# Performance work log

Measured on AMD Instinct MI355X. Metric: run time of the kernel, lower is better.

The kernel has to match this reference:

```python
import jax, jax.numpy as jnp
import numpy as np

N = 65536        # gaussians
NTILE = 8        # tiles per side
TS = 64          # tile size in pixels
T = NTILE * NTILE
K = 256          # depth-sorted gaussians per tile
W = H = NTILE * TS


def setup_inputs() -> dict:
    key = jax.random.key(0)
    ks = jax.random.split(key, 6)
    mu = jax.random.uniform(ks[0], (N, 2), dtype=jnp.float32) * W   # 2D screen means
    L = jax.random.normal(ks[1], (N, 2, 2), dtype=jnp.float32) * 2.0
    # PSD 2x2 covariances with a few-pixel footprint
    cov2d = jnp.einsum('nij,nkj->nik', L, L) + 4.0 * jnp.eye(2, dtype=jnp.float32)
    opacity = jax.random.uniform(ks[2], (N,), dtype=jnp.float32)
    color = jax.random.uniform(ks[3], (N, 3), dtype=jnp.float32)
    depth = jax.random.uniform(ks[4], (N,), dtype=jnp.float32)
    idx = jax.random.randint(ks[5], (T, K), 0, N)
    # depth-sort gaussians within each tile (Screen.depth_sort)
    order = jnp.argsort(depth[idx], axis=1)
    tile_idx = jnp.take_along_axis(idx, order, axis=1).astype(jnp.int32)
    return {"mu": mu, "cov2d": cov2d, "opacity": opacity, "color": color,
            "tile_idx": tile_idx}


def _rasterize(mu, cov2d, opacity, color, tile_idx):
    # closed-form 2x2 inverse of cov2d
    a = cov2d[:, 0, 0]; b = cov2d[:, 0, 1]
    c = cov2d[:, 1, 0]; d = cov2d[:, 1, 1]
    det = jnp.maximum(a * d - b * c, 1e-6)
    inv = jnp.stack([jnp.stack([d, -b], -1),
                     jnp.stack([-c, a], -1)], -2) / det[:, None, None]  # [N,2,2]

    ly, lx = jnp.meshgrid(jnp.arange(TS), jnp.arange(TS), indexing='ij')
    local = (jnp.stack([lx, ly], -1).reshape(TS * TS, 2).astype(jnp.float32)
             + 0.5)  # pixel centers within a tile, [P,2]

    def tile_fn(args):
        tid, idx = args
        ty = tid // NTILE
        tx = tid % NTILE
        origin = jnp.stack([tx * TS, ty * TS]).astype(jnp.float32)
        pix = local + origin                              # [P,2]
        m = mu[idx]                                       # [K,2]
        ic = inv[idx]                                     # [K,2,2]
        op = opacity[idx]                                 # [K]
        col = color[idx]                                  # [K,3]
        dlt = pix[:, None, :] - m[None, :, :]             # [P,K,2]
        maha = jnp.einsum('pki,kij,pkj->pk', dlt, ic, dlt)
        prob = jnp.exp(-0.5 * maha)                       # [P,K]
        alpha = jnp.clip(op[None, :] * prob, 0.01, 0.99)
        # weight_i = alpha_i * (1 - sum_{j<i} alpha_j)  (shifted cumsum, as in source)
        trans = 1.0 - (jnp.cumsum(alpha, axis=1) - alpha)
        w = alpha * trans                                 # [P,K]
        return (w @ col).reshape(TS, TS, 3)

    tiles = jax.lax.map(tile_fn, (jnp.arange(T, dtype=jnp.int32), tile_idx))  # [T,TS,TS,3]
    img = tiles.reshape(NTILE, NTILE, TS, TS, 3)
    img = img.transpose(0, 2, 1, 3, 4).reshape(H, W, 3)
    return img


def reference(mu, cov2d, opacity, color, tile_idx):
    return _rasterize(mu, cov2d, opacity, color, tile_idx)
```

## Files before the change

### kernel.cpp

```cpp
#include <hip/hip_runtime.h>
#include <math.h>

#define TS 64
#define T 64
#define K 256
#define NSEG 4
#define KSEG 64
#define IMG_W 512

__global__ __launch_bounds__(512, 4) void render_all(
    const float* __restrict__ mu, const float* __restrict__ cov,
    const float* __restrict__ opacity, const float* __restrict__ color,
    const int* __restrict__ tile_idx, float* __restrict__ out) {
  __shared__ float4 sA[K];
  __shared__ float4 sB[K];
  __shared__ float sC[K];
  __shared__ float sR[K];
  __shared__ float4 sbuf[2 * K];
  __shared__ float4 sPA[K + 1];
  __shared__ float4 sPK[K + 1];
  __shared__ float sS[NSEG][128][4];
  __shared__ float sD[3][128][4][3];

  int tid = threadIdx.x;
  int blk = blockIdx.x;
  int tile = blk & 63;
  int chunk = blk >> 6;

  if (tid < K) {
    int n = tile_idx[tile * K + tid];
    float a = cov[4 * n + 0];
    float b = cov[4 * n + 1];
    float c = cov[4 * n + 2];
    float d = cov[4 * n + 3];
    float det = fmaxf(a * d - b * c, 1e-6f);
    const float LOG2E = 1.4426950408889634f;
    float s = -0.5f * LOG2E / det;
    float mx = mu[2 * n], my = mu[2 * n + 1];
    float lop = log2f(fmaxf(opacity[n], 1e-30f));
    float cr = color[3 * n], cg = color[3 * n + 1], cb = color[3 * n + 2];
    sA[tid] = make_float4(mx, my, s * d, -s * (b + c));
    sB[tid] = make_float4(s * a, lop, cr, cg);
    sC[tid] = cb;
    float r2 = 1.3862943611f * (lop + 6.6438561898f) * (a + d);
    sR[tid] = r2 * 1.0001f + 1e-3f;
    sbuf[tid] = make_float4(cr, cg, cb, 0.f);
    float fk = (float)tid;
    sbuf[K + tid] = make_float4(fk * cr, fk * cg, fk * cb, 0.f);
  }
  __syncthreads();

  int lane256 = tid & 255;
  float4* mybuf = sbuf + (tid & 256);
  for (int off = 1; off < K; off <<= 1) {
    float4 t;
    bool act = lane256 >= off;
    if (act) t = mybuf[lane256 - off];
    __syncthreads();
    if (act) {
      float4 u = mybuf[lane256];
      mybuf[lane256] = make_float4(u.x + t.x, u.y + t.y, u.z + t.z, 0.f);
    }
    __syncthreads();
  }
  if (tid < K) {
    sPA[tid + 1] = sbuf[tid];
  } else {
    sPK[lane256 + 1] = sbuf[K + lane256];
  }
  if (tid == 0) {
    sPA[0] = make_float4(0.f, 0.f, 0.f, 0.f);
    sPK[0] = make_float4(0.f, 0.f, 0.f, 0.f);
  }
  __syncthreads();

  int seg = __builtin_amdgcn_readfirstlane(tid >> 7);
  int pslot = tid & 127;
  int lx = pslot & 63;
  int bnd = __builtin_amdgcn_readfirstlane(chunk * 2 + ((tid >> 6) & 1));
  int ty = tile >> 3, tx = tile & 7;
  int ly0 = bnd * 4;
  float px = (float)(tx * TS + lx) + 0.5f;
  float py0 = (float)(ty * TS + ly0) + 0.5f;
  const int kb = seg * KSEG;

  unsigned long long m;
  {
    int l = tid & 63;
    float4 Ag = sA[kb + l];
    float r2 = sR[kb + l];
    float x0 = tx * TS + 0.5f, x1 = tx * TS + 63.5f;
    float y0 = py0, y1 = py0 + 3.0f;
    float dxm = fmaxf(fmaxf(Ag.x - x1, x0 - Ag.x), 0.f);
    float dym = fmaxf(fmaxf(Ag.y - y1, y0 - Ag.y), 0.f);
    float d2 = fmaf(dxm, dxm, dym * dym);
    m = __ballot(d2 < r2);
  }

  float C[4][3] = {};
  float An[4][3] = {};
  float Af[3] = {0.f, 0.f, 0.f};
  float S[4] = {};

  int i = kb;
  while (true) {
    int j = (m != 0ULL) ? (kb + (int)__builtin_ctzll(m)) : (kb + KSEG);
    if (j > i) {
      float len = (float)(j - i);
      float4 paj = sPA[j], pai = sPA[i];
      float4 pkj = sPK[j], pki = sPK[i];
      float P1r = paj.x - pai.x, P1g = paj.y - pai.y, P1b = paj.z - pai.z;
      float fi = (float)i;
      float Rr = -1e-4f * fmaf(-fi, P1r, pkj.x - pki.x);
      float Rg = -1e-4f * fmaf(-fi, P1g, pkj.y - pki.y);
      float Rb = -1e-4f * fmaf(-fi, P1b, pkj.z - pki.z);
      Af[0] = fmaf(0.01f, P1r, Af[0]);
      Af[1] = fmaf(0.01f, P1g, Af[1]);
      Af[2] = fmaf(0.01f, P1b, Af[2]);
#pragma unroll
      for (int p = 0; p < 4; ++p) {
        float t = fmaf(-0.01f, S[p], 0.01f);
        C[p][0] = fmaf(t, P1r, C[p][0]) + Rr;
        C[p][1] = fmaf(t, P1g, C[p][1]) + Rg;
        C[p][2] = fmaf(t, P1b, C[p][2]) + Rb;
        S[p] = fmaf(0.01f, len, S[p]);
      }
    }
    if (j >= kb + KSEG) break;
    float4 A4 = sA[j];
    float4 B4 = sB[j];
    float cbv = sC[j];
    float dx = px - A4.x;
    float tb = A4.w * dx;
    float base = fmaf(A4.z * dx, dx, B4.y);
    float dy = py0 - A4.y;
#pragma unroll
    for (int p = 0; p < 4; ++p) {
      float dyp = dy + (float)p;
      float mm = fmaf(dyp, fmaf(B4.x, dyp, tb), base);
      float al =
          __builtin_amdgcn_fmed3f(__builtin_amdgcn_exp2f(mm), 0.01f, 0.99f);
      float w = fmaf(-al, S[p], al);
      C[p][0] = fmaf(w, B4.z, C[p][0]);
      C[p][1] = fmaf(w, B4.w, C[p][1]);
      C[p][2] = fmaf(w, cbv, C[p][2]);
      An[p][0] = fmaf(al, B4.z, An[p][0]);
      An[p][1] = fmaf(al, B4.w, An[p][1]);
      An[p][2] = fmaf(al, cbv, An[p][2]);
      S[p] += al;
    }
    m &= (m - 1ULL);
    i = j + 1;
  }

#pragma unroll
  for (int p = 0; p < 4; ++p) sS[seg][pslot][p] = S[p];
  __syncthreads();

  if (seg >= 1) {
#pragma unroll
    for (int p = 0; p < 4; ++p) {
      float Sp = sS[0][pslot][p];
      if (seg >= 2) Sp += sS[1][pslot][p];
      if (seg >= 3) Sp += sS[2][pslot][p];
      sD[seg - 1][pslot][p][0] = fmaf(-Sp, An[p][0] + Af[0], C[p][0]);
      sD[seg - 1][pslot][p][1] = fmaf(-Sp, An[p][1] + Af[1], C[p][1]);
      sD[seg - 1][pslot][p][2] = fmaf(-Sp, An[p][2] + Af[2], C[p][2]);
    }
  }
  __syncthreads();

  if (seg == 0) {
    int x = tx * TS + lx;
#pragma unroll
    for (int p = 0; p < 4; ++p) {
      int y = ty * TS + ly0 + p;
      size_t o = ((size_t)y * IMG_W + x) * 3;
      out[o + 0] = C[p][0] + sD[0][pslot][p][0] + sD[1][pslot][p][0] +
                   sD[2][pslot][p][0];
      out[o + 1] = C[p][1] + sD[0][pslot][p][1] + sD[1][pslot][p][1] +
                   sD[2][pslot][p][1];
      out[o + 2] = C[p][2] + sD[0][pslot][p][2] + sD[1][pslot][p][2] +
                   sD[2][pslot][p][2];
    }
  }
}

extern "C" void kernel_launch(void* const* d_in, const int* in_sizes, int n_in,
                              void* d_out, int out_size, void* d_ws,
                              size_t ws_size, hipStream_t stream) {
  const float* mu = (const float*)d_in[0];
  const float* cov = (const float*)d_in[1];
  const float* opacity = (const float*)d_in[2];
  const float* color = (const float*)d_in[3];
  const int* tile_idx = (const int*)d_in[4];
  float* out = (float*)d_out;
  (void)d_ws;
  (void)ws_size;

  render_all<<<T * 8, 512, 0, stream>>>(mu, cov, opacity, color, tile_idx,
                                        out);
}
```

Baseline: 68.87 us.

## Replace block-wide shared-memory prefix scan with per-wave shuffle scans

Drops the 8-step block-wide Hillis-Steele scan, which used many __syncthreads, in favour of a per-segment 64-wide wavefront shuffle scan over the color prefixes. Prefix values are then fetched by __shfl inside the gap-accumulation branch instead of being read from shared memory. Work is also split so that the upper 256 threads load colors, with vectorized float4/float2 global loads. The cost is extra shuffle instructions inside the sparse loop and redundant scans across waves.

```diff
diff --git a/kernel.cpp b/kernel.cpp
--- a/kernel.cpp
+++ b/kernel.cpp
@@ -13,12 +13,9 @@
     const float* __restrict__ opacity, const float* __restrict__ color,
     const int* __restrict__ tile_idx, float* __restrict__ out) {
   __shared__ float4 sA[K];
-  __shared__ float4 sB[K];
-  __shared__ float sC[K];
+  __shared__ float2 sB[K];
+  __shared__ float4 sCol[K];
   __shared__ float sR[K];
-  __shared__ float4 sbuf[2 * K];
-  __shared__ float4 sPA[K + 1];
-  __shared__ float4 sPK[K + 1];
   __shared__ float sS[NSEG][128][4];
   __shared__ float sD[3][128][4][3];
 
@@ -27,55 +24,31 @@
   int tile = blk & 63;
   int chunk = blk >> 6;
 
-  if (tid < K) {
-    int n = tile_idx[tile * K + tid];
-    float a = cov[4 * n + 0];
-    float b = cov[4 * n + 1];
-    float c = cov[4 * n + 2];
-    float d = cov[4 * n + 3];
-    float det = fmaxf(a * d - b * c, 1e-6f);
-    const float LOG2E = 1.4426950408889634f;
-    float s = -0.5f * LOG2E / det;
-    float mx = mu[2 * n], my = mu[2 * n + 1];
-    float lop = log2f(fmaxf(opacity[n], 1e-30f));
-    float cr = color[3 * n], cg = color[3 * n + 1], cb = color[3 * n + 2];
-    sA[tid] = make_float4(mx, my, s * d, -s * (b + c));
-    sB[tid] = make_float4(s * a, lop, cr, cg);
-    sC[tid] = cb;
-    float r2 = 1.3862943611f * (lop + 6.6438561898f) * (a + d);
-    sR[tid] = r2 * 1.0001f + 1e-3f;
-    sbuf[tid] = make_float4(cr, cg, cb, 0.f);
-    float fk = (float)tid;
-    sbuf[K + tid] = make_float4(fk * cr, fk * cg, fk * cb, 0.f);
-  }
-  __syncthreads();
-
-  int lane256 = tid & 255;
-  float4* mybuf = sbuf + (tid & 256);
-  for (int off = 1; off < K; off <<= 1) {
-    float4 t;
-    bool act = lane256 >= off;
-    if (act) t = mybuf[lane256 - off];
-    __syncthreads();
-    if (act) {
-      float4 u = mybuf[lane256];
-      mybuf[lane256] = make_float4(u.x + t.x, u.y + t.y, u.z + t.z, 0.f);
-    }
-    __syncthreads();
-  }
-  if (tid < K) {
-    sPA[tid + 1] = sbuf[tid];
-  } else {
-    sPK[lane256 + 1] = sbuf[K + lane256];
-  }
-  if (tid == 0) {
-    sPA[0] = make_float4(0.f, 0.f, 0.f, 0.f);
-    sPK[0] = make_float4(0.f, 0.f, 0.f, 0.f);
+  {
+    int g = tid & 255;
+    int n = tile_idx[tile * K + g];
+    if (tid < K) {
+      float4 cv = *(const float4*)(cov + 4 * n);
+      float2 mm = *(const float2*)(mu + 2 * n);
+      float op = opacity[n];
+      float det = fmaxf(cv.x * cv.w - cv.y * cv.z, 1e-6f);
+      const float LOG2E = 1.4426950408889634f;
+      float s = -0.5f * LOG2E / det;
+      float lop = log2f(fmaxf(op, 1e-30f));
+      sA[g] = make_float4(mm.x, mm.y, s * cv.w, -s * (cv.y + cv.z));
+      sB[g] = make_float2(s * cv.x, lop);
+      float r2 = 1.3862943611f * (lop + 6.6438561898f) * (cv.x + cv.w);
+      sR[g] = r2 * 1.0001f + 1e-3f;
+    } else {
+      const float* cp = color + 3 * n;
+      sCol[g] = make_float4(cp[0], cp[1], cp[2], 0.f);
+    }
   }
   __syncthreads();
 
   int seg = __builtin_amdgcn_readfirstlane(tid >> 7);
   int pslot = tid & 127;
+  int lane = tid & 63;
   int lx = pslot & 63;
   int bnd = __builtin_amdgcn_readfirstlane(chunk * 2 + ((tid >> 6) & 1));
   int ty = tile >> 3, tx = tile & 7;
@@ -84,11 +57,39 @@
   float py0 = (float)(ty * TS + ly0) + 0.5f;
   const int kb = seg * KSEG;
 
+  float icr, icg, icb, jcr, jcg, jcb;
+  {
+    float4 cl = sCol[kb + lane];
+    float fl = (float)lane;
+    icr = cl.x;
+    icg = cl.y;
+    icb = cl.z;
+    jcr = fl * cl.x;
+    jcg = fl * cl.y;
+    jcb = fl * cl.z;
+    for (int off = 1; off < 64; off <<= 1) {
+      float t0 = __shfl_up(icr, off);
+      float t1 = __shfl_up(icg, off);
+      float t2 = __shfl_up(icb, off);
+      float t3 = __shfl_up(jcr, off);
+      float t4 = __shfl_up(jcg, off);
+      float t5 = __shfl_up(jcb, off);
+      if (lane >= off) {
+        icr += t0;
+        icg += t1;
+        icb += t2;
+        jcr += t3;
+        jcg += t4;
+        jcb += t5;
+      }
+    }
+  }
+#define PFX(v, q) ((q) == 0 ? 0.f : __shfl((v), (q)-1))
+
   unsigned long long m;
   {
-    int l = tid & 63;
-    float4 Ag = sA[kb + l];
-    float r2 = sR[kb + l];
+    float4 Ag = sA[kb + lane];
+    float r2 = sR[kb + lane];
     float x0 = tx * TS + 0.5f, x1 = tx * TS + 63.5f;
     float y0 = py0, y1 = py0 + 3.0f;
     float dxm = fmaxf(fmaxf(Ag.x - x1, x0 - Ag.x), 0.f);
@@ -106,14 +107,15 @@
   while (true) {
     int j = (m != 0ULL) ? (kb + (int)__builtin_ctzll(m)) : (kb + KSEG);
     if (j > i) {
-      float len = (float)(j - i);
-      float4 paj = sPA[j], pai = sPA[i];
-      float4 pkj = sPK[j], pki = sPK[i];
-      float P1r = paj.x - pai.x, P1g = paj.y - pai.y, P1b = paj.z - pai.z;
-      float fi = (float)i;
-      float Rr = -1e-4f * fmaf(-fi, P1r, pkj.x - pki.x);
-      float Rg = -1e-4f * fmaf(-fi, P1g, pkj.y - pki.y);
-      float Rb = -1e-4f * fmaf(-fi, P1b, pkj.z - pki.z);
+      int i2 = i - kb, j2 = j - kb;
+      float len = (float)(j2 - i2);
+      float P1r = PFX(icr, j2) - PFX(icr, i2);
+      float P1g = PFX(icg, j2) - PFX(icg, i2);
+      float P1b = PFX(icb, j2) - PFX(icb, i2);
+      float fi = (float)i2;
+      float Rr = -1e-4f * fmaf(-fi, P1r, PFX(jcr, j2) - PFX(jcr, i2));
+      float Rg = -1e-4f * fmaf(-fi, P1g, PFX(jcg, j2) - PFX(jcg, i2));
+      float Rb = -1e-4f * fmaf(-fi, P1b, PFX(jcb, j2) - PFX(jcb, i2));
       Af[0] = fmaf(0.01f, P1r, Af[0]);
       Af[1] = fmaf(0.01f, P1g, Af[1]);
       Af[2] = fmaf(0.01f, P1b, Af[2]);
@@ -128,25 +130,25 @@
     }
     if (j >= kb + KSEG) break;
     float4 A4 = sA[j];
-    float4 B4 = sB[j];
-    float cbv = sC[j];
+    float2 B2 = sB[j];
+    float4 c4 = sCol[j];
     float dx = px - A4.x;
     float tb = A4.w * dx;
-    float base = fmaf(A4.z * dx, dx, B4.y);
+    float base = fmaf(A4.z * dx, dx, B2.y);
     float dy = py0 - A4.y;
 #pragma unroll
     for (int p = 0; p < 4; ++p) {
       float dyp = dy + (float)p;
-      float mm = fmaf(dyp, fmaf(B4.x, dyp, tb), base);
+      float mm = fmaf(dyp, fmaf(B2.x, dyp, tb), base);
       float al =
           __builtin_amdgcn_fmed3f(__builtin_amdgcn_exp2f(mm), 0.01f, 0.99f);
       float w = fmaf(-al, S[p], al);
-      C[p][0] = fmaf(w, B4.z, C[p][0]);
-      C[p][1] = fmaf(w, B4.w, C[p][1]);
-      C[p][2] = fmaf(w, cbv, C[p][2]);
-      An[p][0] = fmaf(al, B4.z, An[p][0]);
-      An[p][1] = fmaf(al, B4.w, An[p][1]);
-      An[p][2] = fmaf(al, cbv, An[p][2]);
+      C[p][0] = fmaf(w, c4.x, C[p][0]);
+      C[p][1] = fmaf(w, c4.y, C[p][1]);
+      C[p][2] = fmaf(w, c4.z, C[p][2]);
+      An[p][0] = fmaf(al, c4.x, An[p][0]);
+      An[p][1] = fmaf(al, c4.y, An[p][1]);
+      An[p][2] = fmaf(al, c4.z, An[p][2]);
       S[p] += al;
     }
     m &= (m - 1ULL);
```

New measurement: 69.79 us. No clear change (+1.3%).
